# Performance work log

Hardware: AMD Instinct MI355X
Metric: run time of the kernel (lower is better)

The kernel has to match this reference:

```python
import jax, jax.numpy as jnp
import numpy as np

N_NODES = 16384
H = 128


def setup_inputs() -> dict:
    key = jax.random.key(0)
    k1, k2, k3, k4, k5 = jax.random.split(key, 5)
    neighbour_h = jax.random.normal(k1, (N_NODES, 2, H), dtype=jnp.float32)
    A = jax.random.uniform(k2, (H, H, 3 * H), dtype=jnp.float32)  # th.rand
    U1_w = jax.random.normal(k3, (3 * H, H), dtype=jnp.float32)   # Linear weight (out,in), no bias
    U2_w = jax.random.normal(k4, (3 * H, H), dtype=jnp.float32)
    U2_b = jax.random.normal(k5, (3 * H,), dtype=jnp.float32)
    return {"neighbour_h": neighbour_h, "A": A, "U1_w": U1_w, "U2_w": U2_w, "U2_b": U2_b}


def reference(neighbour_h, A, U1_w, U2_w, U2_b):
    # compute_iou_gate of BinaryFullTensorCell (pos_stationarity=False)
    n, _, h = neighbour_h.shape
    h1 = neighbour_h[:, 0, :]  # (n, h)
    h2 = neighbour_h[:, 1, :]  # (n, h)
    # bilinear: einsum('ijk,ni,nj->nk') -- contract via per-node outer product
    # then a single GEMM against A reshaped to (h*h, 3h).
    outer = h1[:, :, None] * h2[:, None, :]          # (n, h, h)
    bil = outer.reshape(n, h * h) @ A.reshape(h * h, -1)  # (n, 3h)
    # torch Linear: x @ W.T (+ b)
    out = bil + h1 @ U1_w.T + h2 @ U2_w.T + U2_b
    return out
```

## Files before the change

### kernel.cpp

```cpp
#include <hip/hip_runtime.h>
#include <hip/hip_bf16.h>

typedef __attribute__((ext_vector_type(8))) short bf16x8;
typedef __attribute__((ext_vector_type(16))) float f32x16;
typedef __attribute__((ext_vector_type(4))) float f32x4;
typedef __attribute__((ext_vector_type(4))) unsigned int uint4v;
typedef unsigned short ushort_t;
typedef unsigned int uint_t;

#define N_NODES 16384
#define HD 128
#define NOUT 384
#define PART_ELEMS 6291456

static __device__ __forceinline__ ushort_t f2bf(float f) {
  __hip_bfloat16 b = __float2bfloat16(f);
  return *reinterpret_cast<ushort_t*>(&b);
}

__global__ void prep_all(const float* __restrict__ A, const float* __restrict__ U1,
                         const float* __restrict__ U2, const float* __restrict__ nh,
                         ushort_t* __restrict__ pk, ushort_t* __restrict__ h1,
                         ushort_t* __restrict__ h2, float* __restrict__ h1tf) {
  __shared__ __align__(16) char smem[49152];
  const int b = blockIdx.x;
  const int t = threadIdx.x;

  if (b < 260) {
    short* spk = reinterpret_cast<short*>(smem);
    const int half = b & 1;
    const int gg = t >> 5, ll = t & 31;
    if (b < 256) {
      const int it = b >> 1;
      const size_t krow0 = (size_t)it * 128 + half * 64;
#pragma unroll 4
      for (int kl = 0; kl < 64; ++kl) {
        float v = A[(krow0 + kl) * NOUT + t];
        int cl = kl >> 4, oc = (kl >> 3) & 1, j = kl & 7;
        spk[(gg * 8 + cl * 2 + oc) * 256 + ll * 8 + j] = f2bf(v);
      }
    } else {
      const int u = (b - 256) >> 1;
      const float* U = u ? U2 : U1;
#pragma unroll 4
      for (int kl = 0; kl < 64; ++kl) {
        float v = U[(size_t)t * HD + half * 64 + kl];
        int cl = kl >> 4, oc = (kl >> 3) & 1, j = kl & 7;
        spk[(gg * 8 + cl * 2 + oc) * 256 + ll * 8 + j] = f2bf(v);
      }
    }
    __syncthreads();
    const int it_out = (b < 256) ? (b >> 1) : (128 + ((b - 256) >> 1));
    const int f = t * 64;
    const int g = f >> 11;
    const int inner = f & 2047;
    ushort_t* dst = pk + (size_t)it_out * 49152 + g * 4096 + half * 2048 + inner;
    const uint4* src = reinterpret_cast<const uint4*>(spk + f);
    uint4* d4 = reinterpret_cast<uint4*>(dst);
#pragma unroll
    for (int q = 0; q < 8; ++q) d4[q] = src[q];
  } else {
    if (t < 256) {
      float (*sm)[65] = reinterpret_cast<float(*)[65]>(smem);
      const int g = b - 260;
      const int mt = g & 255, jt = g >> 8;
      const int tx = t & 63, ty = t >> 6;
      const int m0 = mt * 64, j0 = jt * 64;
#pragma unroll
      for (int s = 0; s < 16; ++s) {
        int mm = ty + s * 4;
        float f1 = nh[(size_t)(m0 + mm) * 256 + j0 + tx];
        float f2 = nh[(size_t)(m0 + mm) * 256 + 128 + j0 + tx];
        h1[(size_t)(m0 + mm) * HD + j0 + tx] = f2bf(f1);
        h2[(size_t)(m0 + mm) * HD + j0 + tx] = f2bf(f2);
        sm[mm][tx] = f1;
      }
      __syncthreads();
#pragma unroll
      for (int s = 0; s < 16; ++s) {
        int jj = ty + s * 4;
        h1tf[(size_t)(j0 + jj) * N_NODES + m0 + tx] = sm[tx][jj];
      }
    }
  }
}

#define PK_STEP 98304
#define SLICE_B 17408

#define STAGE(IT, R)                                                              \
  do {                                                                            \
    const char* s_ = pkbase + (size_t)(IT) * PK_STEP;                             \
    char* d_ = ldsb + (R) * SLICE_B;                                              \
    __builtin_amdgcn_global_load_lds((const uint_t*)(s_ + stg),                   \
                                     (uint_t*)(d_ + wv * 1024), 16, 0, 0);        \
    __builtin_amdgcn_global_load_lds((const uint_t*)(s_ + 8192 + stg),            \
                                     (uint_t*)(d_ + 8192 + wv * 1024), 16, 0, 0); \
    const int ith_ = (IT) < 128 ? (IT) : 127;                                     \
    const char* h_ = reinterpret_cast<const char*>(                               \
                         h1tf + (size_t)ith_ * N_NODES + Mt * 256) + wv * 128;    \
    if (lane < 8)                                                                 \
      __builtin_amdgcn_global_load_lds((const uint_t*)(h_ + lane * 16),           \
                                       (uint_t*)(d_ + 16384 + wv * 128), 16, 0, 0); \
  } while (0)

#define READ_NEXT(BBN, SN0, SN1, RN)                                              \
  do {                                                                            \
    const char* lb_ = ldsb + (RN) * SLICE_B;                                      \
    const char* bb_ = lb_ + wn * 8192 + oct * 512 + l31 * 16;                     \
    _Pragma("unroll")                                                             \
    for (int c = 0; c < 8; ++c)                                                   \
      BBN[c] = *reinterpret_cast<const uint4v*>(bb_ + c * 1024);                  \
    SN0 = *reinterpret_cast<const float*>(lb_ + 16384 + (wm * 64 + l31) * 4);     \
    SN1 = *reinterpret_cast<const float*>(lb_ + 16384 + (wm * 64 + 32 + l31) * 4);\
  } while (0)

#define CHAIN(BBC, PC0, PC1)                                                      \
  do {                                                                            \
    PC0 = vz; PC1 = vz;                                                           \
    __builtin_amdgcn_s_setprio(1);                                                \
    _Pragma("unroll")                                                             \
    for (int c = 0; c < 8; ++c) {                                                 \
      bf16x8 f_ = __builtin_bit_cast(bf16x8, BBC[c]);                             \
      PC0 = __builtin_amdgcn_mfma_f32_32x32x16_bf16(                              \
          f_, __builtin_bit_cast(bf16x8, h2u[0][c]), PC0, 0, 0, 0);               \
      PC1 = __builtin_amdgcn_mfma_f32_32x32x16_bf16(                              \
          f_, __builtin_bit_cast(bf16x8, h2u[1][c]), PC1, 0, 0, 0);               \
    }                                                                             \
    __builtin_amdgcn_s_setprio(0);                                                \
  } while (0)

#define TAIL(S0_, S1_, PP0, PP1)                                                  \
  do {                                                                            \
    _Pragma("unroll")                                                             \
    for (int rr = 0; rr < 16; ++rr) {                                             \
      acc[0][rr] += (S0_) * PP0[rr];                                              \
      acc[1][rr] += (S1_) * PP1[rr];                                              \
    }                                                                             \
  } while (0)

__global__ __launch_bounds__(512, 2)
void gemm_kernel(const ushort_t* __restrict__ pk, const ushort_t* __restrict__ h1bf,
                 const ushort_t* __restrict__ h2bf, const float* __restrict__ h1tf,
                 const float* __restrict__ u2b, float* __restrict__ part) {
  __shared__ __align__(16) char ldsb[3 * SLICE_B];

  const int tid = threadIdx.x;
  const int bid = blockIdx.x;
  const int v  = (bid & 7) * 96 + (bid >> 3);
  const int Mt = v & 63;
  const int q  = v >> 6;
  const int Nt = q >> 1;
  const int ks = q & 1;

  const int lane = tid & 63, wv = tid >> 6;
  const int l31 = lane & 31, oct = lane >> 5;
  const int wm = wv >> 1, wn = wv & 1;
  const int mbase = Mt * 256 + wm * 64;
  const int n0w = Nt * 64 + wn * 32;
  const int g0 = Nt * 2;

  uint4v h2u[2][8];
#pragma unroll
  for (int ms = 0; ms < 2; ++ms) {
    const ushort_t* hp = h2bf + (size_t)(mbase + ms * 32 + l31) * HD + oct * 8;
#pragma unroll
    for (int c = 0; c < 8; ++c)
      h2u[ms][c] = *reinterpret_cast<const uint4v*>(hp + c * 16);
  }

  f32x16 acc[2];
  if (ks) {
#pragma unroll
    for (int qq = 0; qq < 4; ++qq) {
      f32x4 bq = *reinterpret_cast<const f32x4*>(u2b + n0w + 8 * qq + 4 * oct);
#pragma unroll
      for (int j = 0; j < 4; ++j) { acc[0][qq * 4 + j] = bq[j]; acc[1][qq * 4 + j] = bq[j]; }
    }
  } else {
    acc[0] = (f32x16)(0.0f);
    acc[1] = (f32x16)(0.0f);
  }

  const int it0 = ks ? 65 : 0;
  const int it1 = ks ? 128 : 65;

  const char* pkbase = reinterpret_cast<const char*>(pk) + (size_t)g0 * 8192;
  const int stg = wv * 1024 + lane * 16;

  const f32x16 vz = (f32x16)(0.0f);

  STAGE(it0, 0);
  STAGE(it0 + 1, 1);
  asm volatile("s_waitcnt vmcnt(3)" ::: "memory");
  __builtin_amdgcn_s_barrier();
  uint4v bbX[8], bbY[8];
  f32x16 pX0, pX1, pY0 = vz, pY1 = vz;
  float sX0, sX1, sY0 = 0.0f, sY1 = 0.0f;
  READ_NEXT(bbX, sX0, sX1, 0);

  int rn = 1, rsb = 2;
  for (int it = it0; it < it1 - 1; it += 2) {
    {
      const float t0 = sY0, t1 = sY1;
      STAGE(it + 2, rsb); rsb = (rsb == 2) ? 0 : rsb + 1;
      asm volatile("s_waitcnt vmcnt(3)" ::: "memory");
      __builtin_amdgcn_s_barrier();
      READ_NEXT(bbY, sY0, sY1, rn); rn = (rn == 2) ? 0 : rn + 1;
      TAIL(t0, t1, pY0, pY1);
      CHAIN(bbX, pX0, pX1);
    }
    {
      const float t0 = sX0, t1 = sX1;
      STAGE(it + 3, rsb); rsb = (rsb == 2) ? 0 : rsb + 1;
      asm volatile("s_waitcnt vmcnt(3)" ::: "memory");
      __builtin_amdgcn_s_barrier();
      READ_NEXT(bbX, sX0, sX1, rn); rn = (rn == 2) ? 0 : rn + 1;
      TAIL(t0, t1, pX0, pX1);
      CHAIN(bbY, pY0, pY1);
    }
  }
  {
    STAGE(it1 + 1, rsb);
    asm volatile("s_waitcnt vmcnt(3)" ::: "memory");
    __builtin_amdgcn_s_barrier();
    TAIL(sY0, sY1, pY0, pY1);
    CHAIN(bbX, pX0, pX1);
    TAIL(sX0, sX1, pX0, pX1);
  }

  if (ks) {
    const char* bt = reinterpret_cast<const char*>(pk) +
                     (size_t)128 * PK_STEP + (size_t)((g0 + wn) * 16 + oct) * 512 +
                     (size_t)l31 * 16;
#pragma unroll
    for (int c = 0; c < 8; ++c) {
      bf16x8 bfr = __builtin_bit_cast(bf16x8, *reinterpret_cast<const uint4v*>(bt + c * 1024));
#pragma unroll
      for (int ms = 0; ms < 2; ++ms) {
        bf16x8 a = *reinterpret_cast<const bf16x8*>(
            h1bf + (size_t)(mbase + ms * 32 + l31) * HD + c * 16 + oct * 8);
        acc[ms] = __builtin_amdgcn_mfma_f32_32x32x16_bf16(bfr, a, acc[ms], 0, 0, 0);
      }
    }
    const char* bt2 = bt + PK_STEP;
#pragma unroll
    for (int c = 0; c < 8; ++c) {
      bf16x8 bfr = __builtin_bit_cast(bf16x8, *reinterpret_cast<const uint4v*>(bt2 + c * 1024));
#pragma unroll
      for (int ms = 0; ms < 2; ++ms) {
        acc[ms] = __builtin_amdgcn_mfma_f32_32x32x16_bf16(
            bfr, __builtin_bit_cast(bf16x8, h2u[ms][c]), acc[ms], 0, 0, 0);
      }
    }
  }

  float* my = part + (size_t)ks * PART_ELEMS;
#pragma unroll
  for (int ms = 0; ms < 2; ++ms) {
    float* rowp = my + (size_t)(mbase + ms * 32 + l31) * NOUT + n0w + 4 * oct;
#pragma unroll
    for (int qq = 0; qq < 4; ++qq) {
      f32x4 o;
      o[0] = acc[ms][qq * 4 + 0];
      o[1] = acc[ms][qq * 4 + 1];
      o[2] = acc[ms][qq * 4 + 2];
      o[3] = acc[ms][qq * 4 + 3];
      *reinterpret_cast<f32x4*>(rowp + 8 * qq) = o;
    }
  }
}

__global__ void reduce2(const float* __restrict__ part, float* __restrict__ out) {
  int i = blockIdx.x * 256 + threadIdx.x;
  float4 a = reinterpret_cast<const float4*>(part)[i];
  float4 b = reinterpret_cast<const float4*>(part + PART_ELEMS)[i];
  float4 o;
  o.x = a.x + b.x; o.y = a.y + b.y; o.z = a.z + b.z; o.w = a.w + b.w;
  reinterpret_cast<float4*>(out)[i] = o;
}

extern "C" void kernel_launch(void* const* d_in, const int* in_sizes, int n_in,
                              void* d_out, int out_size, void* d_ws, size_t ws_size,
                              hipStream_t stream) {
  const float* nh  = (const float*)d_in[0];
  const float* A   = (const float*)d_in[1];
  const float* U1  = (const float*)d_in[2];
  const float* U2  = (const float*)d_in[3];
  const float* U2b = (const float*)d_in[4];

  char* ws = (char*)d_ws;
  ushort_t* pk   = (ushort_t*)(ws);
  ushort_t* h1bf = (ushort_t*)(ws + 12779520);
  ushort_t* h2bf = (ushort_t*)(ws + 16973824);
  float*    h1tf = (float*)(ws + 21168128);
  float*    part = (float*)(ws + 29556736);

  prep_all<<<dim3(772), 384, 0, stream>>>(A, U1, U2, nh, pk, h1bf, h2bf, h1tf);
  gemm_kernel<<<dim3(768), 512, 0, stream>>>(pk, h1bf, h2bf, h1tf, U2b, part);
  reduce2<<<dim3(6144), 256, 0, stream>>>(part, (float*)d_out);
}
```

Baseline: 292.2 us.

## Deepen LDS staging pipeline to six slices with one barrier per iteration pair

Grows the LDS ring buffer from three to six slices, prefetching six K-steps ahead, and restructures the main loop so each pair of iterations uses a single barrier instead of two. LDS reads for the next steps are interleaved after each MFMA chain. The goal is to hide more global-load latency and cut synchronisation. In exchange, LDS per block roughly doubles (about 104KB), which can threaten the two-blocks-per-CU occupancy.

```diff
diff --git a/kernel.cpp b/kernel.cpp
--- a/kernel.cpp
+++ b/kernel.cpp
@@ -104,7 +104,7 @@
                                        (uint_t*)(d_ + 16384 + wv * 128), 16, 0, 0); \
   } while (0)
 
-#define READ_NEXT(BBN, SN0, SN1, RN)                                              \
+#define READN(BBN, SN0, SN1, RN)                                                  \
   do {                                                                            \
     const char* lb_ = ldsb + (RN) * SLICE_B;                                      \
     const char* bb_ = lb_ + wn * 8192 + oct * 512 + l31 * 16;                     \
@@ -143,7 +143,7 @@
 void gemm_kernel(const ushort_t* __restrict__ pk, const ushort_t* __restrict__ h1bf,
                  const ushort_t* __restrict__ h2bf, const float* __restrict__ h1tf,
                  const float* __restrict__ u2b, float* __restrict__ part) {
-  __shared__ __align__(16) char ldsb[3 * SLICE_B];
+  __shared__ __align__(16) char ldsb[6 * SLICE_B];
 
   const int tid = threadIdx.x;
   const int bid = blockIdx.x;
@@ -190,41 +190,46 @@
 
   const f32x16 vz = (f32x16)(0.0f);
 
-  STAGE(it0, 0);
+  STAGE(it0 + 0, 0);
   STAGE(it0 + 1, 1);
-  asm volatile("s_waitcnt vmcnt(3)" ::: "memory");
+  STAGE(it0 + 2, 2);
+  STAGE(it0 + 3, 3);
+  STAGE(it0 + 4, 4);
+  STAGE(it0 + 5, 5);
+  asm volatile("s_waitcnt vmcnt(12)" ::: "memory");
   __builtin_amdgcn_s_barrier();
   uint4v bbX[8], bbY[8];
   f32x16 pX0, pX1, pY0 = vz, pY1 = vz;
-  float sX0, sX1, sY0 = 0.0f, sY1 = 0.0f;
-  READ_NEXT(bbX, sX0, sX1, 0);
-
-  int rn = 1, rsb = 2;
-  for (int it = it0; it < it1 - 1; it += 2) {
-    {
-      const float t0 = sY0, t1 = sY1;
-      STAGE(it + 2, rsb); rsb = (rsb == 2) ? 0 : rsb + 1;
-      asm volatile("s_waitcnt vmcnt(3)" ::: "memory");
-      __builtin_amdgcn_s_barrier();
-      READ_NEXT(bbY, sY0, sY1, rn); rn = (rn == 2) ? 0 : rn + 1;
-      TAIL(t0, t1, pY0, pY1);
-      CHAIN(bbX, pX0, pX1);
-    }
-    {
-      const float t0 = sX0, t1 = sX1;
-      STAGE(it + 3, rsb); rsb = (rsb == 2) ? 0 : rsb + 1;
-      asm volatile("s_waitcnt vmcnt(3)" ::: "memory");
-      __builtin_amdgcn_s_barrier();
-      READ_NEXT(bbX, sX0, sX1, rn); rn = (rn == 2) ? 0 : rn + 1;
-      TAIL(t0, t1, pX0, pX1);
-      CHAIN(bbY, pY0, pY1);
-    }
+  float sX0, sX1, sY0, sY1;
+  READN(bbX, sX0, sX1, 0);
+  READN(bbY, sY0, sY1, 1);
+  float tyO0 = 0.0f, tyO1 = 0.0f;
+
+  int sb = 0;
+  for (int it = it0; it + 1 < it1; it += 2) {
+    const int st0 = sb, st1 = sb + 1;
+    const int rd0 = (sb + 2 >= 6) ? sb - 4 : sb + 2;
+    const int rd1 = (sb + 3 >= 6) ? sb - 3 : sb + 3;
+
+    asm volatile("s_waitcnt lgkmcnt(0)" ::: "memory");
+    asm volatile("s_waitcnt vmcnt(6)" ::: "memory");
+    __builtin_amdgcn_s_barrier();
+
+    STAGE(it + 6, st0);
+    TAIL(tyO0, tyO1, pY0, pY1);
+    const float cx0 = sX0, cx1 = sX1;
+    CHAIN(bbX, pX0, pX1);
+    READN(bbX, sX0, sX1, rd0);
+    STAGE(it + 7, st1);
+    tyO0 = sY0; tyO1 = sY1;
+    CHAIN(bbY, pY0, pY1);
+    READN(bbY, sY0, sY1, rd1);
+    TAIL(cx0, cx1, pX0, pX1);
+
+    sb += 2; if (sb == 6) sb = 0;
   }
   {
-    STAGE(it1 + 1, rsb);
-    asm volatile("s_waitcnt vmcnt(3)" ::: "memory");
-    __builtin_amdgcn_s_barrier();
-    TAIL(sY0, sY1, pY0, pY1);
+    TAIL(tyO0, tyO1, pY0, pY1);
     CHAIN(bbX, pX0, pX1);
     TAIL(sX0, sX1, pX0, pX1);
   }
```

Measured after the change: 305.3 us. +4.5%, slower.

## Halve GEMM block M-tile, double grid, and interleave LDS reads with MFMA chain

Applied to the files above, without the earlier changes.

Shrinks the gemm block from 8 to 4 waves, giving each block 128 rows instead of 256 and launching twice as many blocks. Each wave now stages four 16-byte chunks per slice, and the waitcnt thresholds are adjusted to match. The next slice's LDS reads are fused into the MFMA chain loop so loads overlap compute, the setprio hints are dropped, and the dead final stage in the epilogue is removed. In exchange, each staged A-slice is now reused by half as many rows, which doubles global traffic for the packed weights per node.

```diff
diff --git a/kernel.cpp b/kernel.cpp
--- a/kernel.cpp
+++ b/kernel.cpp
@@ -86,39 +86,56 @@
 }
 
 #define PK_STEP 98304
-#define SLICE_B 17408
+#define SLICE_B 16896
 
 #define STAGE(IT, R)                                                              \
   do {                                                                            \
-    const char* s_ = pkbase + (size_t)(IT) * PK_STEP;                             \
-    char* d_ = ldsb + (R) * SLICE_B;                                              \
-    __builtin_amdgcn_global_load_lds((const uint_t*)(s_ + stg),                   \
-                                     (uint_t*)(d_ + wv * 1024), 16, 0, 0);        \
-    __builtin_amdgcn_global_load_lds((const uint_t*)(s_ + 8192 + stg),            \
-                                     (uint_t*)(d_ + 8192 + wv * 1024), 16, 0, 0); \
+    const char* s_ = pkbase + (size_t)(IT) * PK_STEP + stg;                       \
+    char* d_ = ldsb + (R) * SLICE_B + wv * 4096;                                  \
+    __builtin_amdgcn_global_load_lds((const uint_t*)(s_),        (uint_t*)(d_),        16, 0, 0); \
+    __builtin_amdgcn_global_load_lds((const uint_t*)(s_ + 1024), (uint_t*)(d_ + 1024), 16, 0, 0); \
+    __builtin_amdgcn_global_load_lds((const uint_t*)(s_ + 2048), (uint_t*)(d_ + 2048), 16, 0, 0); \
+    __builtin_amdgcn_global_load_lds((const uint_t*)(s_ + 3072), (uint_t*)(d_ + 3072), 16, 0, 0); \
     const int ith_ = (IT) < 128 ? (IT) : 127;                                     \
     const char* h_ = reinterpret_cast<const char*>(                               \
-                         h1tf + (size_t)ith_ * N_NODES + Mt * 256) + wv * 128;    \
+                         h1tf + (size_t)ith_ * N_NODES + Mt * 128) + wv * 128;    \
     if (lane < 8)                                                                 \
       __builtin_amdgcn_global_load_lds((const uint_t*)(h_ + lane * 16),           \
-                                       (uint_t*)(d_ + 16384 + wv * 128), 16, 0, 0); \
-  } while (0)
-
-#define READ_NEXT(BBN, SN0, SN1, RN)                                              \
+          (uint_t*)(ldsb + (R) * SLICE_B + 16384 + wv * 128), 16, 0, 0);          \
+  } while (0)
+
+#define READN(BBN, SN0, SN1, RN)                                                  \
   do {                                                                            \
     const char* lb_ = ldsb + (RN) * SLICE_B;                                      \
     const char* bb_ = lb_ + wn * 8192 + oct * 512 + l31 * 16;                     \
+    SN0 = *reinterpret_cast<const float*>(lb_ + 16384 + (wm * 64 + l31) * 4);     \
+    SN1 = *reinterpret_cast<const float*>(lb_ + 16384 + (wm * 64 + 32 + l31) * 4);\
     _Pragma("unroll")                                                             \
     for (int c = 0; c < 8; ++c)                                                   \
       BBN[c] = *reinterpret_cast<const uint4v*>(bb_ + c * 1024);                  \
+  } while (0)
+
+#define CHAINRD(BBC, PC0, PC1, BBN, SN0, SN1, RN)                                 \
+  do {                                                                            \
+    const char* lb_ = ldsb + (RN) * SLICE_B;                                      \
+    const char* bb_ = lb_ + wn * 8192 + oct * 512 + l31 * 16;                     \
     SN0 = *reinterpret_cast<const float*>(lb_ + 16384 + (wm * 64 + l31) * 4);     \
     SN1 = *reinterpret_cast<const float*>(lb_ + 16384 + (wm * 64 + 32 + l31) * 4);\
+    PC0 = vz; PC1 = vz;                                                           \
+    _Pragma("unroll")                                                             \
+    for (int c = 0; c < 8; ++c) {                                                 \
+      BBN[c] = *reinterpret_cast<const uint4v*>(bb_ + c * 1024);                  \
+      bf16x8 f_ = __builtin_bit_cast(bf16x8, BBC[c]);                             \
+      PC0 = __builtin_amdgcn_mfma_f32_32x32x16_bf16(                              \
+          f_, __builtin_bit_cast(bf16x8, h2u[0][c]), PC0, 0, 0, 0);               \
+      PC1 = __builtin_amdgcn_mfma_f32_32x32x16_bf16(                              \
+          f_, __builtin_bit_cast(bf16x8, h2u[1][c]), PC1, 0, 0, 0);               \
+    }                                                                             \
   } while (0)
 
 #define CHAIN(BBC, PC0, PC1)                                                      \
   do {                                                                            \
     PC0 = vz; PC1 = vz;                                                           \
-    __builtin_amdgcn_s_setprio(1);                                                \
     _Pragma("unroll")                                                             \
     for (int c = 0; c < 8; ++c) {                                                 \
       bf16x8 f_ = __builtin_bit_cast(bf16x8, BBC[c]);                             \
@@ -127,7 +144,6 @@
       PC1 = __builtin_amdgcn_mfma_f32_32x32x16_bf16(                              \
           f_, __builtin_bit_cast(bf16x8, h2u[1][c]), PC1, 0, 0, 0);               \
     }                                                                             \
-    __builtin_amdgcn_s_setprio(0);                                                \
   } while (0)
 
 #define TAIL(S0_, S1_, PP0, PP1)                                                  \
@@ -139,7 +155,7 @@
     }                                                                             \
   } while (0)
 
-__global__ __launch_bounds__(512, 2)
+__global__ __launch_bounds__(256, 2)
 void gemm_kernel(const ushort_t* __restrict__ pk, const ushort_t* __restrict__ h1bf,
                  const ushort_t* __restrict__ h2bf, const float* __restrict__ h1tf,
                  const float* __restrict__ u2b, float* __restrict__ part) {
@@ -147,16 +163,16 @@
 
   const int tid = threadIdx.x;
   const int bid = blockIdx.x;
-  const int v  = (bid & 7) * 96 + (bid >> 3);
-  const int Mt = v & 63;
-  const int q  = v >> 6;
+  const int v  = (bid & 7) * 192 + (bid >> 3);
+  const int Mt = v & 127;
+  const int q  = v >> 7;
   const int Nt = q >> 1;
   const int ks = q & 1;
 
   const int lane = tid & 63, wv = tid >> 6;
   const int l31 = lane & 31, oct = lane >> 5;
   const int wm = wv >> 1, wn = wv & 1;
-  const int mbase = Mt * 256 + wm * 64;
+  const int mbase = Mt * 128 + wm * 64;
   const int n0w = Nt * 64 + wn * 32;
   const int g0 = Nt * 2;
 
@@ -186,44 +202,39 @@
   const int it1 = ks ? 128 : 65;
 
   const char* pkbase = reinterpret_cast<const char*>(pk) + (size_t)g0 * 8192;
-  const int stg = wv * 1024 + lane * 16;
+  const int stg = wv * 4096 + lane * 16;
 
   const f32x16 vz = (f32x16)(0.0f);
 
   STAGE(it0, 0);
   STAGE(it0 + 1, 1);
-  asm volatile("s_waitcnt vmcnt(3)" ::: "memory");
+  asm volatile("s_waitcnt vmcnt(5)" ::: "memory");
   __builtin_amdgcn_s_barrier();
   uint4v bbX[8], bbY[8];
   f32x16 pX0, pX1, pY0 = vz, pY1 = vz;
   float sX0, sX1, sY0 = 0.0f, sY1 = 0.0f;
-  READ_NEXT(bbX, sX0, sX1, 0);
+  READN(bbX, sX0, sX1, 0);
 
   int rn = 1, rsb = 2;
-  for (int it = it0; it < it1 - 1; it += 2) {
+  for (int it = it0; it + 1 < it1; it += 2) {
     {
       const float t0 = sY0, t1 = sY1;
       STAGE(it + 2, rsb); rsb = (rsb == 2) ? 0 : rsb + 1;
-      asm volatile("s_waitcnt vmcnt(3)" ::: "memory");
+      asm volatile("s_waitcnt vmcnt(5)" ::: "memory");
       __builtin_amdgcn_s_barrier();
-      READ_NEXT(bbY, sY0, sY1, rn); rn = (rn == 2) ? 0 : rn + 1;
+      CHAINRD(bbX, pX0, pX1, bbY, sY0, sY1, rn); rn = (rn == 2) ? 0 : rn + 1;
       TAIL(t0, t1, pY0, pY1);
-      CHAIN(bbX, pX0, pX1);
     }
     {
       const float t0 = sX0, t1 = sX1;
       STAGE(it + 3, rsb); rsb = (rsb == 2) ? 0 : rsb + 1;
-      asm volatile("s_waitcnt vmcnt(3)" ::: "memory");
+      asm volatile("s_waitcnt vmcnt(5)" ::: "memory");
       __builtin_amdgcn_s_barrier();
-      READ_NEXT(bbX, sX0, sX1, rn); rn = (rn == 2) ? 0 : rn + 1;
+      CHAINRD(bbY, pY0, pY1, bbX, sX0, sX1, rn); rn = (rn == 2) ? 0 : rn + 1;
       TAIL(t0, t1, pX0, pX1);
-      CHAIN(bbY, pY0, pY1);
     }
   }
   {
-    STAGE(it1 + 1, rsb);
-    asm volatile("s_waitcnt vmcnt(3)" ::: "memory");
-    __builtin_amdgcn_s_barrier();
     TAIL(sY0, sY1, pY0, pY1);
     CHAIN(bbX, pX0, pX1);
     TAIL(sX0, sX1, pX0, pX1);
@@ -297,6 +308,6 @@
   float*    part = (float*)(ws + 29556736);
 
   prep_all<<<dim3(772), 384, 0, stream>>>(A, U1, U2, nh, pk, h1bf, h2bf, h1tf);
-  gemm_kernel<<<dim3(768), 512, 0, stream>>>(pk, h1bf, h2bf, h1tf, U2b, part);
+  gemm_kernel<<<dim3(1536), 256, 0, stream>>>(pk, h1bf, h2bf, h1tf, U2b, part);
   reduce2<<<dim3(6144), 256, 0, stream>>>(part, (float*)d_out);
 }
```

Result: no change. 292.4 us (+0.1%).
